# Performance work log

Hardware: AMD Instinct MI355X
Metric: run time of the kernel (lower is better)

The kernel has to match this reference:

```python
import jax, jax.numpy as jnp
from jax import lax
import numpy as np

GAMMA = 0.1      # sinkhorn_alpha
EPS = 0.005      # stop_thr
MAXITERS = 1000  # OT_max_iter
TINY = 1e-30


def _pairwise_sq_dist(x, y):
    return (jnp.sum(x * x, axis=1, keepdims=True)
            + jnp.sum(y * y, axis=1)[None, :]
            - 2.0 * (x @ y.T))


def _sinkhorn(M, r, c):
    # M: (B,H,W); r: (1,H); c: (1,W). Faithful to _sinkhorn_inline.
    r_ = r[:, :, None]          # (1,H,1)
    c_ = c[:, None, :]          # (1,W,1 -> 1,1,W)
    M_min = jnp.min(M, axis=2, keepdims=True)
    P0 = jnp.exp(-GAMMA * (M - M_min))

    def cond(state):
        _, err, it = state
        return (err > EPS) & (it < MAXITERS)

    def body(state):
        P, _, it = state
        alpha = jnp.sum(P, axis=2, keepdims=True)
        P1 = P / jnp.maximum(alpha, TINY) * r_
        beta = jnp.sum(P1, axis=1, keepdims=True)
        err = jnp.max(jnp.sum(jnp.abs(beta - c_), axis=2))
        P2 = P1 / jnp.maximum(beta, TINY) * c_
        # torch breaks BEFORE the column update when converged -> keep P1 then
        Pn = jnp.where(err <= EPS, P1, P2)
        return Pn, err, it + 1

    init = (P0, jnp.asarray(jnp.inf, M.dtype), jnp.asarray(0, jnp.int32))
    P, _, _ = lax.while_loop(cond, body, init)
    return P


def setup_inputs() -> dict:
    key = jax.random.key(0)
    k1, k2 = jax.random.split(key)
    x = jax.random.normal(k1, (1024, 512), dtype=jnp.float32)
    y = jax.random.normal(k2, (16384, 512), dtype=jnp.float32)
    return {"x": x, "y": y}


def reference(x, y):
    M = _pairwise_sq_dist(x, y)           # (n, m)
    n, m = M.shape
    # init_a_dist / init_b_dist are None -> uniform marginals (already normalized)
    a = jnp.full((1, n), 1.0 / n, dtype=M.dtype)
    b = jnp.full((1, m), 1.0 / m, dtype=M.dtype)
    # n <= m by construction -> implicit path takes the non-transpose branch
    P = _sinkhorn(M[None], a, b)[0]       # (n, m)
    loss_ETP = jnp.sum(P * M)
    return loss_ETP, P
```

## Files before the change

kernel.cpp:

```cpp
#include <hip/hip_runtime.h>

#define N_ROWS 1024
#define M_COLS 16384
#define DIM 512

constexpr float GAMMA_ = 0.1f;
constexpr float INV_GAMMA = 10.0f;
constexpr float EPS_ = 0.005f;
constexpr float TINY_ = 1e-30f;
constexpr float RVAL = 1.0f / 1024.0f;
constexpr float CVAL = 1.0f / 16384.0f;

typedef __attribute__((ext_vector_type(8))) short bf16x8;
typedef __attribute__((ext_vector_type(4))) float f32x4;

__device__ __forceinline__ float waveRedSum(float v) {
#pragma unroll
    for (int o = 32; o > 0; o >>= 1) v += __shfl_down(v, o);
    return v;
}
__device__ __forceinline__ float waveRedMin(float v) {
#pragma unroll
    for (int o = 32; o > 0; o >>= 1) v = fminf(v, __shfl_down(v, o));
    return v;
}

__device__ __forceinline__ unsigned sysloadu(const unsigned* p) {
    return __hip_atomic_load(p, __ATOMIC_RELAXED, __HIP_MEMORY_SCOPE_SYSTEM);
}
__device__ __forceinline__ void sysstoreu(unsigned* p, unsigned v) {
    __hip_atomic_store(p, v, __ATOMIC_RELAXED, __HIP_MEMORY_SCOPE_SYSTEM);
}
__device__ __forceinline__ float sysloadf(const float* p) {
    return __hip_atomic_load(p, __ATOMIC_RELAXED, __HIP_MEMORY_SCOPE_SYSTEM);
}
__device__ __forceinline__ void sysstoref(float* p, float v) {
    __hip_atomic_store(p, v, __ATOMIC_RELAXED, __HIP_MEMORY_SCOPE_SYSTEM);
}

__device__ __forceinline__ void gbarx(unsigned* __restrict__ arr, unsigned* __restrict__ bcast,
                                      int b, int tid, unsigned e) {
    __syncthreads();
    if (tid == 0) sysstoreu(&arr[b], e);
    if (b == 0) {
        if (tid < 256) {
            while (sysloadu(&arr[tid]) < e) __builtin_amdgcn_s_sleep(1);
        }
        __syncthreads();
        if (tid == 0) sysstoreu(bcast, e);
    } else {
        if (tid == 0) {
            while (sysloadu(bcast) < e) __builtin_amdgcn_s_sleep(1);
        }
    }
    __syncthreads();
}

__device__ __forceinline__ unsigned bf16b(float f) {
    unsigned u = __float_as_uint(f);
    return (u + 0x7FFFu + ((u >> 16) & 1u)) >> 16;
}

__global__ void conv_x(const float* __restrict__ X, unsigned short* __restrict__ xh,
                       unsigned short* __restrict__ xl, float* __restrict__ sx) {
    const int row = blockIdx.x, t = threadIdx.x;
    const float* xr = X + (size_t)row * DIM + t * 8;
    float4 a = *(const float4*)xr, c = *(const float4*)(xr + 4);
    float v[8] = {a.x, a.y, a.z, a.w, c.x, c.y, c.z, c.w};
    unsigned hs[8], ls[8];
    float sq = 0.f;
#pragma unroll
    for (int j = 0; j < 8; ++j) {
        unsigned h = bf16b(v[j]);
        hs[j] = h;
        ls[j] = bf16b(v[j] - __uint_as_float(h << 16));
        sq = fmaf(v[j], v[j], sq);
    }
    uint4 hv = make_uint4(hs[0] | (hs[1] << 16), hs[2] | (hs[3] << 16),
                          hs[4] | (hs[5] << 16), hs[6] | (hs[7] << 16));
    uint4 lv = make_uint4(ls[0] | (ls[1] << 16), ls[2] | (ls[3] << 16),
                          ls[4] | (ls[5] << 16), ls[6] | (ls[7] << 16));
    const size_t off = (size_t)row * 1024 + t * 16;
    *(uint4*)((char*)xh + off) = hv;
    *(uint4*)((char*)xl + off) = lv;
    sq = waveRedSum(sq);
    if (t == 0) sx[row] = sq;
}

__global__ void init_state(float* __restrict__ ubuf, unsigned* __restrict__ flags,
                           float* __restrict__ out) {
    int idx = blockIdx.x * blockDim.x + threadIdx.x;
    if (idx < 512) flags[idx] = 0u;
    if (idx < 512) { ubuf[idx * 4] = 1.0f; ubuf[idx * 4 + 1] = 1.0f;
                     ubuf[idx * 4 + 2] = 1.0f; ubuf[idx * 4 + 3] = 1.0f; }
    if (idx == 0) out[0] = 0.0f;
}

__global__ __launch_bounds__(1024, 4) void sinkhorn_full(
        const unsigned short* __restrict__ xh, const unsigned short* __restrict__ xl,
        const float* __restrict__ Y, const float* __restrict__ sx,
        float* __restrict__ ubuf, float* __restrict__ Mming,
        float* __restrict__ out, unsigned* __restrict__ flags) {
    const int tid = threadIdx.x;
    const int b = blockIdx.x;
    const int lane = tid & 63;
    const int w = tid >> 6;
    const int l15 = lane & 15;
    const int q = lane >> 4;
    float* Pbuf = out + 1;
    float* spart2 = out + 10000000;
    unsigned* arr = flags;
    unsigned* bcast = flags + 288;

    __shared__ __align__(16) char ldsY[131072];
    __shared__ float sx_lds[1024];
    __shared__ float mmin_lds[1024];
    __shared__ float u_lds[1024];
    __shared__ float sy_lds[64];
    __shared__ float v_lds[2][64];
    __shared__ float t_acc[16][68];
    __shared__ float srow_lds[16][64];
    __shared__ float red[16];
    __shared__ float sh_err;
    __shared__ float sh_eprev;

    {
        const int row = tid >> 4;
        const int c = tid & 15;
        const float* yr = Y + (size_t)((b << 6) + row) * DIM + c * 32;
        const int swz = (row & 7) << 4;
        float sq = 0.f;
#pragma unroll
        for (int s2 = 0; s2 < 4; ++s2) {
            float4 f0 = *(const float4*)(yr + s2 * 8);
            float4 f1 = *(const float4*)(yr + s2 * 8 + 4);
            float v8[8] = {f0.x, f0.y, f0.z, f0.w, f1.x, f1.y, f1.z, f1.w};
            unsigned h[8], lo[8];
#pragma unroll
            for (int j = 0; j < 8; ++j) {
                h[j] = bf16b(v8[j]);
                lo[j] = bf16b(v8[j] - __uint_as_float(h[j] << 16));
                sq = fmaf(v8[j], v8[j], sq);
            }
            const int off = (row * 1024 + c * 64 + s2 * 16) ^ swz;
            *(uint4*)(ldsY + off) = make_uint4(h[0] | (h[1] << 16), h[2] | (h[3] << 16),
                                               h[4] | (h[5] << 16), h[6] | (h[7] << 16));
            *(uint4*)(ldsY + 65536 + off) = make_uint4(lo[0] | (lo[1] << 16), lo[2] | (lo[3] << 16),
                                                       lo[4] | (lo[5] << 16), lo[6] | (lo[7] << 16));
        }
        float* sy_part = (float*)t_acc;
        sy_part[row * 17 + c] = sq;
        sx_lds[tid] = sx[tid];
        if (tid < 64) { v_lds[0][tid] = 1.0f; v_lds[1][tid] = 1.0f; }
        if (tid == 0) sh_eprev = 0.0f;
    }
    __syncthreads();
    if (tid < 64) {
        const float* sy_part = (const float*)t_acc;
        float s = 0.f;
#pragma unroll
        for (int c2 = 0; c2 < 16; ++c2) s += sy_part[tid * 17 + c2];
        sy_lds[tid] = s;
    }
    __syncthreads();

    f32x4 kf[4][4] = {};
    {
        const int rowbase = (w << 6) + l15;
        const int kofs = q * 8;
#pragma unroll 1
        for (int ks = 0; ks < 16; ++ks) {
            bf16x8 ah[4], al[4], bh[4], bl[4];
#pragma unroll
            for (int i = 0; i < 4; ++i) {
                const size_t xo = (size_t)(rowbase + i * 16) * 512 + ks * 32 + kofs;
                ah[i] = *(const bf16x8*)(xh + xo);
                al[i] = *(const bf16x8*)(xl + xo);
                const int cl = i * 16 + l15;
                const int bo = (cl * 1024 + ks * 64 + q * 16) ^ ((cl & 7) << 4);
                bh[i] = *(const bf16x8*)(ldsY + bo);
                bl[i] = *(const bf16x8*)(ldsY + 65536 + bo);
            }
#pragma unroll
            for (int i = 0; i < 4; ++i)
#pragma unroll
                for (int j = 0; j < 4; ++j) {
                    kf[i][j] = __builtin_amdgcn_mfma_f32_16x16x32_bf16(ah[i], bh[j], kf[i][j], 0, 0, 0);
                    kf[i][j] = __builtin_amdgcn_mfma_f32_16x16x32_bf16(ah[i], bl[j], kf[i][j], 0, 0, 0);
                    kf[i][j] = __builtin_amdgcn_mfma_f32_16x16x32_bf16(al[i], bh[j], kf[i][j], 0, 0, 0);
                }
        }
    }
#pragma unroll
    for (int i = 0; i < 4; ++i)
#pragma unroll
        for (int j = 0; j < 4; ++j) {
            const float syv = sy_lds[j * 16 + l15];
#pragma unroll
            for (int reg = 0; reg < 4; ++reg) {
                const int r = (w << 6) + i * 16 + (q << 2) + reg;
                kf[i][j][reg] = sx_lds[r] + syv - 2.0f * kf[i][j][reg];
            }
        }
    {
        float mn[4][4];
#pragma unroll
        for (int i = 0; i < 4; ++i)
#pragma unroll
            for (int reg = 0; reg < 4; ++reg) {
                float m = fminf(fminf(kf[i][0][reg], kf[i][1][reg]),
                                fminf(kf[i][2][reg], kf[i][3][reg]));
#pragma unroll
                for (int o = 1; o < 16; o <<= 1) m = fminf(m, __shfl_xor(m, o));
                mn[i][reg] = m;
            }
        if (l15 == 0) {
#pragma unroll
            for (int i = 0; i < 4; ++i)
#pragma unroll
                for (int reg = 0; reg < 4; ++reg)
                    srow_lds[w][i * 16 + (q << 2) + reg] = mn[i][reg];
        }
        __syncthreads();
        sysstoref(&spart2[(size_t)b * 1056 + (w << 6) + lane], srow_lds[w][lane]);
    }
    gbarx(arr, bcast, b, tid, 1u);
    if (w >= 1 && w <= 4) {
        const int r = (b << 2) + (w - 1);
        float m = fminf(fminf(sysloadf(&spart2[(size_t)lane * 1056 + r]),
                              sysloadf(&spart2[(size_t)(lane + 64) * 1056 + r])),
                        fminf(sysloadf(&spart2[(size_t)(lane + 128) * 1056 + r]),
                              sysloadf(&spart2[(size_t)(lane + 192) * 1056 + r])));
        m = waveRedMin(m);
        if (lane == 0) sysstoref(&Mming[r], m);
    }
    gbarx(arr, bcast, b, tid, 2u);
    if (tid < 256) {
#pragma unroll
        for (int k2 = 0; k2 < 4; ++k2) mmin_lds[tid * 4 + k2] = sysloadf(&Mming[tid * 4 + k2]);
    }
    __syncthreads();
#pragma unroll
    for (int i = 0; i < 4; ++i)
#pragma unroll
        for (int j = 0; j < 4; ++j)
#pragma unroll
            for (int reg = 0; reg < 4; ++reg) {
                const int r = (w << 6) + i * 16 + (q << 2) + reg;
                kf[i][j][reg] = __expf(-GAMMA_ * (kf[i][j][reg] - mmin_lds[r]));
            }

    int cur = 0, vsel = 0, brk = 0;
    int it = 0;
    for (;; ++it) {
        const unsigned ep = 3u + 2u * (unsigned)it;
        {
            float vv[4];
#pragma unroll
            for (int j = 0; j < 4; ++j) vv[j] = v_lds[cur][j * 16 + l15];
            float rs[4][4];
#pragma unroll
            for (int i = 0; i < 4; ++i)
#pragma unroll
                for (int reg = 0; reg < 4; ++reg) {
                    float pp = kf[i][0][reg] * vv[0];
                    pp = fmaf(kf[i][1][reg], vv[1], pp);
                    pp = fmaf(kf[i][2][reg], vv[2], pp);
                    pp = fmaf(kf[i][3][reg], vv[3], pp);
#pragma unroll
                    for (int o = 1; o < 16; o <<= 1) pp += __shfl_xor(pp, o);
                    rs[i][reg] = pp;
                }
            if (l15 == 0) {
#pragma unroll
                for (int i = 0; i < 4; ++i)
#pragma unroll
                    for (int reg = 0; reg < 4; ++reg)
                        srow_lds[w][i * 16 + (q << 2) + reg] = rs[i][reg];
            }
            __syncthreads();
            sysstoref(&spart2[(size_t)b * 1056 + (w << 6) + lane], srow_lds[w][lane]);
            if (tid == 0) sysstoref(&spart2[(size_t)b * 1056 + 1024], sh_eprev);
        }
        gbarx(arr, bcast, b, tid, ep);
        float* uOld = ubuf + (((it & 1) ^ 1) << 10);
        float* uNew = ubuf + ((it & 1) << 10);
        {
            if (w == 0) {
                float e = 0.f;
                if (it > 0)
                    e = sysloadf(&spart2[(size_t)lane * 1056 + 1024]) +
                        sysloadf(&spart2[(size_t)(lane + 64) * 1056 + 1024]) +
                        sysloadf(&spart2[(size_t)(lane + 128) * 1056 + 1024]) +
                        sysloadf(&spart2[(size_t)(lane + 192) * 1056 + 1024]);
                e = waveRedSum(e);
                if (lane == 0) sh_err = (it > 0) ? e : 1e30f;
            } else if (w <= 4) {
                const int r = (b << 2) + (w - 1);
                float s = sysloadf(&spart2[(size_t)lane * 1056 + r]) +
                          sysloadf(&spart2[(size_t)(lane + 64) * 1056 + r]) +
                          sysloadf(&spart2[(size_t)(lane + 128) * 1056 + r]) +
                          sysloadf(&spart2[(size_t)(lane + 192) * 1056 + r]);
                s = waveRedSum(s);
                if (lane == 0) {
                    float uo = sysloadf(&uOld[r]);
                    sysstoref(&uNew[r], uo * RVAL / fmaxf(uo * s, TINY_));
                }
            }
        }
        __syncthreads();
        float err = sh_err;
        brk = (err <= EPS_) ? 1 : ((it == 1000) ? 2 : 0);
        gbarx(arr, bcast, b, tid, ep + 1u);
        if (brk) { vsel = (brk == 1) ? (cur ^ 1) : cur; break; }
        if (tid < 256) {
#pragma unroll
            for (int k2 = 0; k2 < 4; ++k2) u_lds[tid * 4 + k2] = sysloadf(&uNew[tid * 4 + k2]);
        }
        __syncthreads();
        {
            float uu[4][4];
#pragma unroll
            for (int i = 0; i < 4; ++i)
#pragma unroll
                for (int reg = 0; reg < 4; ++reg)
                    uu[i][reg] = u_lds[(w << 6) + i * 16 + (q << 2) + reg];
            float tj[4];
#pragma unroll
            for (int j = 0; j < 4; ++j) {
                float t = 0.f;
#pragma unroll
                for (int i = 0; i < 4; ++i)
#pragma unroll
                    for (int reg = 0; reg < 4; ++reg)
                        t = fmaf(kf[i][j][reg], uu[i][reg], t);
                t += __shfl_xor(t, 16);
                t += __shfl_xor(t, 32);
                tj[j] = t;
            }
            if (q == 0) {
#pragma unroll
                for (int j = 0; j < 4; ++j) t_acc[w][j * 16 + l15] = tj[j];
            }
        }
        __syncthreads();
        if (tid < 64) {
            float t = 0.f;
#pragma unroll
            for (int w2 = 0; w2 < 16; ++w2) t += t_acc[w2][tid];
            float vc = v_lds[cur][tid];
            float beta = vc * t;
            float e = fabsf(beta - CVAL);
            v_lds[cur ^ 1][tid] = vc * CVAL / fmaxf(beta, TINY_);
            e = waveRedSum(e);
            if (tid == 0) sh_eprev = e;
        }
        __syncthreads();
        cur ^= 1;
    }

    const float* uEpi = ubuf + (((it & 1) ^ 1) << 10);
    if (tid < 256) {
#pragma unroll
        for (int k2 = 0; k2 < 4; ++k2) u_lds[tid * 4 + k2] = sysloadf(&uEpi[tid * 4 + k2]);
    }
    __syncthreads();
    float vv[4];
#pragma unroll
    for (int j = 0; j < 4; ++j) vv[j] = v_lds[vsel][j * 16 + l15];
    float lsum = 0.f;
#pragma unroll
    for (int i = 0; i < 4; ++i)
#pragma unroll
        for (int reg = 0; reg < 4; ++reg) {
            const int r = (w << 6) + i * 16 + (q << 2) + reg;
            const float ur = u_lds[r];
            const float mmr = mmin_lds[r];
            float* prow = Pbuf + (size_t)r * M_COLS + (b << 6) + l15;
#pragma unroll
            for (int j = 0; j < 4; ++j) {
                float kv = kf[i][j][reg];
                float pv = 0.f;
                if (kv > 0.f) {
                    pv = ur * kv * vv[j];
                    lsum = fmaf(pv, mmr - __logf(kv) * INV_GAMMA, lsum);
                }
                prow[j * 16] = pv;
            }
        }
    lsum = waveRedSum(lsum);
    if (lane == 0) red[w] = lsum;
    __syncthreads();
    if (tid == 0) {
        float s = 0.f;
#pragma unroll
        for (int i2 = 0; i2 < 16; ++i2) s += red[i2];
        atomicAdd(out, s);
    }
}

extern "C" void kernel_launch(void* const* d_in, const int* in_sizes, int n_in,
                              void* d_out, int out_size, void* d_ws, size_t ws_size,
                              hipStream_t stream) {
    const float* x = (const float*)d_in[0];
    const float* y = (const float*)d_in[1];
    float* out = (float*)d_out;
    float* ws = (float*)d_ws;
    float* sx    = ws;
    float* Mming = ws + 1024;
    float* ubuf  = ws + 2048;
    unsigned* flags = (unsigned*)(ws + 4096);

    unsigned short* xh = (unsigned short*)(out + 300000);
    unsigned short* xl = (unsigned short*)(out + 600000);

    conv_x<<<N_ROWS, 64, 0, stream>>>(x, xh, xl, sx);
    init_state<<<2, 256, 0, stream>>>(ubuf, flags, out);
    {
        const unsigned short *xhc = xh, *xlc = xl;
        const float *yc = y, *sxc = sx;
        void* args[] = {(void*)&xhc, (void*)&xlc, (void*)&yc, (void*)&sxc,
                        (void*)&ubuf, (void*)&Mming, (void*)&out, (void*)&flags};
        hipLaunchCooperativeKernel((const void*)sinkhorn_full, dim3(256), dim3(1024), args, 0, stream);
    }
}
```

Baseline: 208.5 us.

## Replace global barriers with tagged-value dataflow sync and distributed row reductions

Removes the two-phase centralized grid barrier (gather at block 0, then broadcast) that ran twice per Sinkhorn iteration. Instead, each block publishes its partial column sums and a per-block arrival flag, 16 reducer blocks wait on the flags, compute u for 64 rows each, and publish it as epoch-tagged 64-bit values. Consumers spin directly on those tags, so each iteration needs one synchronisation point instead of two. The u update is kept in registers on the reducer blocks, the partial-sum layout is transposed for contiguous reads, and the epilogue uses the previous u copy saved in LDS. The cost is more spinning on many tagged words and more careful epoch and double-buffer logic, which raises the risk of ordering bugs.

```diff
diff --git a/kernel.cpp b/kernel.cpp
--- a/kernel.cpp
+++ b/kernel.cpp
@@ -13,17 +13,13 @@
 
 typedef __attribute__((ext_vector_type(8))) short bf16x8;
 typedef __attribute__((ext_vector_type(4))) float f32x4;
+typedef unsigned long long u64;
 
 __device__ __forceinline__ float waveRedSum(float v) {
 #pragma unroll
     for (int o = 32; o > 0; o >>= 1) v += __shfl_down(v, o);
     return v;
 }
-__device__ __forceinline__ float waveRedMin(float v) {
-#pragma unroll
-    for (int o = 32; o > 0; o >>= 1) v = fminf(v, __shfl_down(v, o));
-    return v;
-}
 
 __device__ __forceinline__ unsigned sysloadu(const unsigned* p) {
     return __hip_atomic_load(p, __ATOMIC_RELAXED, __HIP_MEMORY_SCOPE_SYSTEM);
@@ -37,23 +33,11 @@
 __device__ __forceinline__ void sysstoref(float* p, float v) {
     __hip_atomic_store(p, v, __ATOMIC_RELAXED, __HIP_MEMORY_SCOPE_SYSTEM);
 }
-
-__device__ __forceinline__ void gbarx(unsigned* __restrict__ arr, unsigned* __restrict__ bcast,
-                                      int b, int tid, unsigned e) {
-    __syncthreads();
-    if (tid == 0) sysstoreu(&arr[b], e);
-    if (b == 0) {
-        if (tid < 256) {
-            while (sysloadu(&arr[tid]) < e) __builtin_amdgcn_s_sleep(1);
-        }
-        __syncthreads();
-        if (tid == 0) sysstoreu(bcast, e);
-    } else {
-        if (tid == 0) {
-            while (sysloadu(bcast) < e) __builtin_amdgcn_s_sleep(1);
-        }
-    }
-    __syncthreads();
+__device__ __forceinline__ u64 sysloadu64(const u64* p) {
+    return __hip_atomic_load(p, __ATOMIC_RELAXED, __HIP_MEMORY_SCOPE_SYSTEM);
+}
+__device__ __forceinline__ void sysstoreu64(u64* p, u64 v) {
+    __hip_atomic_store(p, v, __ATOMIC_RELAXED, __HIP_MEMORY_SCOPE_SYSTEM);
 }
 
 __device__ __forceinline__ unsigned bf16b(float f) {
@@ -87,20 +71,23 @@
     if (t == 0) sx[row] = sq;
 }
 
-__global__ void init_state(float* __restrict__ ubuf, unsigned* __restrict__ flags,
+__global__ void init_state(unsigned* __restrict__ arr, u64* __restrict__ utag,
+                           u64* __restrict__ mmintag, u64* __restrict__ errtot,
                            float* __restrict__ out) {
     int idx = blockIdx.x * blockDim.x + threadIdx.x;
-    if (idx < 512) flags[idx] = 0u;
-    if (idx < 512) { ubuf[idx * 4] = 1.0f; ubuf[idx * 4 + 1] = 1.0f;
-                     ubuf[idx * 4 + 2] = 1.0f; ubuf[idx * 4 + 3] = 1.0f; }
+    if (idx < 256) arr[idx] = 0u;
+    if (idx < 2048) utag[idx] = 0ull;
+    if (idx < 1024) mmintag[idx] = 0ull;
+    if (idx < 4) errtot[idx] = 0ull;
     if (idx == 0) out[0] = 0.0f;
 }
 
-__global__ __launch_bounds__(1024, 4) void sinkhorn_full(
+__global__ __launch_bounds__(1024) void sinkhorn_full(
         const unsigned short* __restrict__ xh, const unsigned short* __restrict__ xl,
         const float* __restrict__ Y, const float* __restrict__ sx,
-        float* __restrict__ ubuf, float* __restrict__ Mming,
-        float* __restrict__ out, unsigned* __restrict__ flags) {
+        float* __restrict__ out, unsigned* __restrict__ arr,
+        u64* __restrict__ utag, u64* __restrict__ mmintag,
+        u64* __restrict__ errtot, float* __restrict__ err_p) {
     const int tid = threadIdx.x;
     const int b = blockIdx.x;
     const int lane = tid & 63;
@@ -109,13 +96,12 @@
     const int q = lane >> 4;
     float* Pbuf = out + 1;
     float* spart2 = out + 10000000;
-    unsigned* arr = flags;
-    unsigned* bcast = flags + 288;
 
     __shared__ __align__(16) char ldsY[131072];
     __shared__ float sx_lds[1024];
     __shared__ float mmin_lds[1024];
     __shared__ float u_lds[1024];
+    __shared__ float u_prev_lds[1024];
     __shared__ float sy_lds[64];
     __shared__ float v_lds[2][64];
     __shared__ float t_acc[16][68];
@@ -123,6 +109,8 @@
     __shared__ float red[16];
     __shared__ float sh_err;
     __shared__ float sh_eprev;
+
+    float u_prev = 1.0f;
 
     {
         const int row = tid >> 4;
@@ -222,22 +210,33 @@
                     srow_lds[w][i * 16 + (q << 2) + reg] = mn[i][reg];
         }
         __syncthreads();
-        sysstoref(&spart2[(size_t)b * 1056 + (w << 6) + lane], srow_lds[w][lane]);
-    }
-    gbarx(arr, bcast, b, tid, 1u);
-    if (w >= 1 && w <= 4) {
-        const int r = (b << 2) + (w - 1);
-        float m = fminf(fminf(sysloadf(&spart2[(size_t)lane * 1056 + r]),
-                              sysloadf(&spart2[(size_t)(lane + 64) * 1056 + r])),
-                        fminf(sysloadf(&spart2[(size_t)(lane + 128) * 1056 + r]),
-                              sysloadf(&spart2[(size_t)(lane + 192) * 1056 + r])));
-        m = waveRedMin(m);
-        if (lane == 0) sysstoref(&Mming[r], m);
-    }
-    gbarx(arr, bcast, b, tid, 2u);
+        sysstoref(&spart2[(size_t)tid * 256 + b], srow_lds[w][lane]);
+        __syncthreads();
+        if (tid == 0) sysstoreu(&arr[b], 1u);
+    }
+    if (b < 16) {
+        if (tid < 256) { while (sysloadu(&arr[tid]) < 1u) __builtin_amdgcn_s_sleep(1); }
+        __syncthreads();
+        const int lrow = (b << 6) + (w << 2) + q;
+        const float* sp = spart2 + (size_t)lrow * 256 + (l15 << 4);
+        float m = sysloadf(&sp[0]);
+#pragma unroll
+        for (int k = 1; k < 16; ++k) m = fminf(m, sysloadf(&sp[k]));
+        m = fminf(m, __shfl_xor(m, 1));
+        m = fminf(m, __shfl_xor(m, 2));
+        m = fminf(m, __shfl_xor(m, 4));
+        m = fminf(m, __shfl_xor(m, 8));
+        if (l15 == 0)
+            sysstoreu64(&mmintag[lrow], (1ull << 32) | (u64)(unsigned)__float_as_uint(m));
+    }
     if (tid < 256) {
-#pragma unroll
-        for (int k2 = 0; k2 < 4; ++k2) mmin_lds[tid * 4 + k2] = sysloadf(&Mming[tid * 4 + k2]);
+        const u64* ms = mmintag + (tid << 2);
+#pragma unroll
+        for (int k = 0; k < 4; ++k) {
+            u64 e = sysloadu64(&ms[k]);
+            while ((unsigned)(e >> 32) < 1u) { __builtin_amdgcn_s_sleep(1); e = sysloadu64(&ms[k]); }
+            mmin_lds[(tid << 2) + k] = __uint_as_float((unsigned)e);
+        }
     }
     __syncthreads();
 #pragma unroll
@@ -250,10 +249,10 @@
                 kf[i][j][reg] = __expf(-GAMMA_ * (kf[i][j][reg] - mmin_lds[r]));
             }
 
-    int cur = 0, vsel = 0, brk = 0;
+    int cur = 0, vsel = 0;
     int it = 0;
     for (;; ++it) {
-        const unsigned ep = 3u + 2u * (unsigned)it;
+        const unsigned ep = (unsigned)it + 2u;
         {
             float vv[4];
 #pragma unroll
@@ -279,45 +278,64 @@
                         srow_lds[w][i * 16 + (q << 2) + reg] = rs[i][reg];
             }
             __syncthreads();
-            sysstoref(&spart2[(size_t)b * 1056 + (w << 6) + lane], srow_lds[w][lane]);
-            if (tid == 0) sysstoref(&spart2[(size_t)b * 1056 + 1024], sh_eprev);
-        }
-        gbarx(arr, bcast, b, tid, ep);
-        float* uOld = ubuf + (((it & 1) ^ 1) << 10);
-        float* uNew = ubuf + ((it & 1) << 10);
-        {
-            if (w == 0) {
-                float e = 0.f;
-                if (it > 0)
-                    e = sysloadf(&spart2[(size_t)lane * 1056 + 1024]) +
-                        sysloadf(&spart2[(size_t)(lane + 64) * 1056 + 1024]) +
-                        sysloadf(&spart2[(size_t)(lane + 128) * 1056 + 1024]) +
-                        sysloadf(&spart2[(size_t)(lane + 192) * 1056 + 1024]);
+            sysstoref(&spart2[(size_t)tid * 256 + b], srow_lds[w][lane]);
+            if (tid == 0) sysstoref(&err_p[b], sh_eprev);
+            __syncthreads();
+            if (tid == 0) sysstoreu(&arr[b], ep);
+        }
+        if (b < 16) {
+            if (tid < 256) { while (sysloadu(&arr[tid]) < ep) __builtin_amdgcn_s_sleep(1); }
+            __syncthreads();
+            const int lrow = (b << 6) + (w << 2) + q;
+            const float* sp = spart2 + (size_t)lrow * 256 + (l15 << 4);
+            float s = 0.f;
+#pragma unroll
+            for (int k = 0; k < 16; ++k) s += sysloadf(&sp[k]);
+            s += __shfl_xor(s, 1);
+            s += __shfl_xor(s, 2);
+            s += __shfl_xor(s, 4);
+            s += __shfl_xor(s, 8);
+            if (l15 == 0) {
+                float un = u_prev * RVAL / fmaxf(u_prev * s, TINY_);
+                u_prev = un;
+                sysstoreu64(&utag[((it & 1) << 10) + lrow],
+                            ((u64)ep << 32) | (u64)(unsigned)__float_as_uint(un));
+            }
+            if (b == 0 && tid < 256) {
+                float e = sysloadf(&err_p[tid]);
                 e = waveRedSum(e);
-                if (lane == 0) sh_err = (it > 0) ? e : 1e30f;
-            } else if (w <= 4) {
-                const int r = (b << 2) + (w - 1);
-                float s = sysloadf(&spart2[(size_t)lane * 1056 + r]) +
-                          sysloadf(&spart2[(size_t)(lane + 64) * 1056 + r]) +
-                          sysloadf(&spart2[(size_t)(lane + 128) * 1056 + r]) +
-                          sysloadf(&spart2[(size_t)(lane + 192) * 1056 + r]);
-                s = waveRedSum(s);
-                if (lane == 0) {
-                    float uo = sysloadf(&uOld[r]);
-                    sysstoref(&uNew[r], uo * RVAL / fmaxf(uo * s, TINY_));
+                if (lane == 0)
+                    sysstoreu64(&errtot[w], ((u64)ep << 32) | (u64)(unsigned)__float_as_uint(e));
+            }
+        }
+        if (tid < 256) {
+#pragma unroll
+            for (int k = 0; k < 4; ++k) u_prev_lds[(tid << 2) + k] = u_lds[(tid << 2) + k];
+            const u64* us = utag + ((it & 1) << 10) + (tid << 2);
+#pragma unroll
+            for (int k = 0; k < 4; ++k) {
+                u64 e = sysloadu64(&us[k]);
+                while ((unsigned)(e >> 32) < ep) { __builtin_amdgcn_s_sleep(1); e = sysloadu64(&us[k]); }
+                u_lds[(tid << 2) + k] = __uint_as_float((unsigned)e);
+            }
+        }
+        if (tid == 0) {
+            float et = 1e30f;
+            if (it > 0) {
+                et = 0.f;
+#pragma unroll
+                for (int k = 0; k < 4; ++k) {
+                    u64 e = sysloadu64(&errtot[k]);
+                    while ((unsigned)(e >> 32) < ep) { __builtin_amdgcn_s_sleep(1); e = sysloadu64(&errtot[k]); }
+                    et += __uint_as_float((unsigned)e);
                 }
             }
-        }
-        __syncthreads();
-        float err = sh_err;
-        brk = (err <= EPS_) ? 1 : ((it == 1000) ? 2 : 0);
-        gbarx(arr, bcast, b, tid, ep + 1u);
+            sh_err = et;
+        }
+        __syncthreads();
+        const float err = sh_err;
+        const int brk = (err <= EPS_) ? 1 : ((it == 1000) ? 2 : 0);
         if (brk) { vsel = (brk == 1) ? (cur ^ 1) : cur; break; }
-        if (tid < 256) {
-#pragma unroll
-            for (int k2 = 0; k2 < 4; ++k2) u_lds[tid * 4 + k2] = sysloadf(&uNew[tid * 4 + k2]);
-        }
-        __syncthreads();
         {
             float uu[4][4];
 #pragma unroll
@@ -359,12 +377,8 @@
         cur ^= 1;
     }
 
-    const float* uEpi = ubuf + (((it & 1) ^ 1) << 10);
-    if (tid < 256) {
-#pragma unroll
-        for (int k2 = 0; k2 < 4; ++k2) u_lds[tid * 4 + k2] = sysloadf(&uEpi[tid * 4 + k2]);
-    }
     __syncthreads();
+
     float vv[4];
 #pragma unroll
     for (int j = 0; j < 4; ++j) vv[j] = v_lds[vsel][j * 16 + l15];
@@ -374,7 +388,7 @@
 #pragma unroll
         for (int reg = 0; reg < 4; ++reg) {
             const int r = (w << 6) + i * 16 + (q << 2) + reg;
-            const float ur = u_lds[r];
+            const float ur = u_prev_lds[r];
             const float mmr = mmin_lds[r];
             float* prow = Pbuf + (size_t)r * M_COLS + (b << 6) + l15;
 #pragma unroll
@@ -405,22 +419,25 @@
     const float* x = (const float*)d_in[0];
     const float* y = (const float*)d_in[1];
     float* out = (float*)d_out;
-    float* ws = (float*)d_ws;
-    float* sx    = ws;
-    float* Mming = ws + 1024;
-    float* ubuf  = ws + 2048;
-    unsigned* flags = (unsigned*)(ws + 4096);
+    char* wsb = (char*)d_ws;
+    unsigned* arr   = (unsigned*)wsb;
+    u64* utag       = (u64*)(wsb + 1024);
+    u64* mmintag    = (u64*)(wsb + 17408);
+    u64* errtot     = (u64*)(wsb + 25600);
+    float* err_p    = (float*)(wsb + 25632);
+    float* sx       = (float*)(wsb + 26656);
 
     unsigned short* xh = (unsigned short*)(out + 300000);
     unsigned short* xl = (unsigned short*)(out + 600000);
 
     conv_x<<<N_ROWS, 64, 0, stream>>>(x, xh, xl, sx);
-    init_state<<<2, 256, 0, stream>>>(ubuf, flags, out);
+    init_state<<<16, 256, 0, stream>>>(arr, utag, mmintag, errtot, out);
     {
         const unsigned short *xhc = xh, *xlc = xl;
         const float *yc = y, *sxc = sx;
         void* args[] = {(void*)&xhc, (void*)&xlc, (void*)&yc, (void*)&sxc,
-                        (void*)&ubuf, (void*)&Mming, (void*)&out, (void*)&flags};
+                        (void*)&out, (void*)&arr, (void*)&utag, (void*)&mmintag,
+                        (void*)&errtot, (void*)&err_p};
         hipLaunchCooperativeKernel((const void*)sinkhorn_full, dim3(256), dim3(1024), args, 0, stream);
     }
 }
```

Result: slower. 327.8 us (+57.2%).
